# Optimization experiments

Measured on AMD Instinct MI355X. Metric: run time of the kernel, lower is better.

## Reference

```python
import jax, jax.numpy as jnp
import numpy as np

B, D = 256, 1024
MARGIN = 0.2  # contrastive margin


def setup_inputs() -> dict:
    key = jax.random.key(0)
    k_im, k_s = jax.random.split(key)
    im = jax.random.normal(k_im, (B, D), dtype=jnp.float32)
    # s viewed by the torch module as [1, B, B, D]; we pass it as [B, B, D]
    s = jax.random.normal(k_s, (B, B, D), dtype=jnp.float32)
    return {"im": im, "s": s}


def reference(im, s):
    # Torch code broadcasts to an O(B^3*D) intermediate then keeps only
    # M[i, j] = scores[j, i, j] = dot(im[j], s[i, j]).
    # We compute exactly those B^2 dot products directly.
    scores = jnp.einsum('jd,ijd->ij', im, s)  # [B, B]
    diag = jnp.diagonal(scores)               # [B]
    not_eye = ~jnp.eye(scores.shape[0], dtype=bool)
    # cost_s[i,j] = relu(margin + M[i,j] - M[i,i]); cost_im uses column diag
    cost_s = jnp.where(not_eye, jnp.maximum(MARGIN + scores - diag[:, None], 0.0), 0.0)
    cost_im = jnp.where(not_eye, jnp.maximum(MARGIN + scores - diag[None, :], 0.0), 0.0)
    # max_violation=True: hardest negative per row / per column
    cost_s = cost_s.max(axis=1)
    cost_im = cost_im.max(axis=0)
    return cost_s.sum() + cost_im.sum()
```

## Files before the change

### kernel.cpp

```cpp
#include <hip/hip_runtime.h>

#define BSZ 256
#define DDIM 1024
#define MARGIN 0.2f
#define WPB 4
#define PPW 8

__global__ __launch_bounds__(256) void scores_kernel(const float* __restrict__ im,
                                                     const float* __restrict__ s,
                                                     float* __restrict__ scores) {
    const int wave = threadIdx.x >> 6;
    const int lane = threadIdx.x & 63;
    const int w = blockIdx.x * WPB + wave;
    const int j = w & (BSZ - 1);
    const int iBase = (w >> 8) * PPW;

    const float4* ip = reinterpret_cast<const float4*>(im + (size_t)j * DDIM);
    float4 b0 = ip[0 * 64 + lane];
    float4 b1 = ip[1 * 64 + lane];
    float4 b2 = ip[2 * 64 + lane];
    float4 b3 = ip[3 * 64 + lane];

#pragma unroll
    for (int it = 0; it < PPW; ++it) {
        const int p = (iBase + it) * BSZ + j;
        const float4* sp = reinterpret_cast<const float4*>(s + (size_t)p * DDIM);
        float4 a0 = sp[0 * 64 + lane];
        float4 a1 = sp[1 * 64 + lane];
        float4 a2 = sp[2 * 64 + lane];
        float4 a3 = sp[3 * 64 + lane];
        float acc = a0.x * b0.x + a0.y * b0.y + a0.z * b0.z + a0.w * b0.w;
        acc += a1.x * b1.x + a1.y * b1.y + a1.z * b1.z + a1.w * b1.w;
        acc += a2.x * b2.x + a2.y * b2.y + a2.z * b2.z + a2.w * b2.w;
        acc += a3.x * b3.x + a3.y * b3.y + a3.z * b3.z + a3.w * b3.w;
#pragma unroll
        for (int off = 32; off > 0; off >>= 1) acc += __shfl_down(acc, off);
        if (lane == 0) scores[p] = acc;
    }
}

__global__ __launch_bounds__(256) void rowcol_kernel(const float* __restrict__ scores,
                                                     float* __restrict__ partial) {
    const int t = blockIdx.x;
    const int j = threadIdx.x;
    __shared__ float wr[4], wc[4];

    const float dg = scores[t * BSZ + t];
    float rowv = 0.0f, colv = 0.0f;
    if (j != t) {
        rowv = fmaxf(MARGIN + scores[t * BSZ + j] - dg, 0.0f);
        colv = fmaxf(MARGIN + scores[j * BSZ + t] - dg, 0.0f);
    }
#pragma unroll
    for (int off = 32; off > 0; off >>= 1) {
        rowv = fmaxf(rowv, __shfl_down(rowv, off));
        colv = fmaxf(colv, __shfl_down(colv, off));
    }
    const int wave = j >> 6;
    const int lane = j & 63;
    if (lane == 0) { wr[wave] = rowv; wc[wave] = colv; }
    __syncthreads();
    if (j == 0) {
        float rm = fmaxf(fmaxf(wr[0], wr[1]), fmaxf(wr[2], wr[3]));
        float cm = fmaxf(fmaxf(wc[0], wc[1]), fmaxf(wc[2], wc[3]));
        partial[t] = rm + cm;
    }
}

__global__ __launch_bounds__(256) void sum_kernel(const float* __restrict__ partial,
                                                  float* __restrict__ out) {
    const int t = threadIdx.x;
    __shared__ float wsum[4];
    float v = partial[t];
#pragma unroll
    for (int off = 32; off > 0; off >>= 1) v += __shfl_down(v, off);
    if ((t & 63) == 0) wsum[t >> 6] = v;
    __syncthreads();
    if (t == 0) out[0] = wsum[0] + wsum[1] + wsum[2] + wsum[3];
}

extern "C" void kernel_launch(void* const* d_in, const int* in_sizes, int n_in,
                              void* d_out, int out_size, void* d_ws, size_t ws_size,
                              hipStream_t stream) {
    const float* im = (const float*)d_in[0];
    const float* s  = (const float*)d_in[1];
    float* out = (float*)d_out;
    float* scores  = (float*)d_ws;
    float* partial = scores + BSZ * BSZ;

    const int nWaves = (BSZ * BSZ) / PPW;
    scores_kernel<<<nWaves / WPB, 256, 0, stream>>>(im, s, scores);
    rowcol_kernel<<<BSZ, 256, 0, stream>>>(scores, partial);
    sum_kernel<<<1, 256, 0, stream>>>(partial, out);
}
```

Before: 46.94 us.

## Fuse row/col and sum kernels via last-block atomic; use nontemporal loads

Merges the final sum kernel into the row/column epilogue using an atomic counter, so the last finishing block performs the global reduction. It also switches the streaming loads of s to nontemporal loads so they avoid polluting the cache. This removes one kernel launch but adds a memset on the stream and an atomic plus fences per block.

```diff
diff --git a/kernel.cpp b/kernel.cpp
--- a/kernel.cpp
+++ b/kernel.cpp
@@ -5,6 +5,8 @@
 #define MARGIN 0.2f
 #define WPB 4
 #define PPW 8
+
+typedef float f32x4 __attribute__((ext_vector_type(4)));
 
 __global__ __launch_bounds__(256) void scores_kernel(const float* __restrict__ im,
                                                      const float* __restrict__ s,
@@ -15,20 +17,20 @@
     const int j = w & (BSZ - 1);
     const int iBase = (w >> 8) * PPW;
 
-    const float4* ip = reinterpret_cast<const float4*>(im + (size_t)j * DDIM);
-    float4 b0 = ip[0 * 64 + lane];
-    float4 b1 = ip[1 * 64 + lane];
-    float4 b2 = ip[2 * 64 + lane];
-    float4 b3 = ip[3 * 64 + lane];
+    const f32x4* ip = reinterpret_cast<const f32x4*>(im + (size_t)j * DDIM);
+    f32x4 b0 = ip[0 * 64 + lane];
+    f32x4 b1 = ip[1 * 64 + lane];
+    f32x4 b2 = ip[2 * 64 + lane];
+    f32x4 b3 = ip[3 * 64 + lane];
 
 #pragma unroll
     for (int it = 0; it < PPW; ++it) {
         const int p = (iBase + it) * BSZ + j;
-        const float4* sp = reinterpret_cast<const float4*>(s + (size_t)p * DDIM);
-        float4 a0 = sp[0 * 64 + lane];
-        float4 a1 = sp[1 * 64 + lane];
-        float4 a2 = sp[2 * 64 + lane];
-        float4 a3 = sp[3 * 64 + lane];
+        const f32x4* sp = reinterpret_cast<const f32x4*>(s + (size_t)p * DDIM);
+        f32x4 a0 = __builtin_nontemporal_load(&sp[0 * 64 + lane]);
+        f32x4 a1 = __builtin_nontemporal_load(&sp[1 * 64 + lane]);
+        f32x4 a2 = __builtin_nontemporal_load(&sp[2 * 64 + lane]);
+        f32x4 a3 = __builtin_nontemporal_load(&sp[3 * 64 + lane]);
         float acc = a0.x * b0.x + a0.y * b0.y + a0.z * b0.z + a0.w * b0.w;
         acc += a1.x * b1.x + a1.y * b1.y + a1.z * b1.z + a1.w * b1.w;
         acc += a2.x * b2.x + a2.y * b2.y + a2.z * b2.z + a2.w * b2.w;
@@ -39,11 +41,16 @@
     }
 }
 
-__global__ __launch_bounds__(256) void rowcol_kernel(const float* __restrict__ scores,
-                                                     float* __restrict__ partial) {
+__global__ __launch_bounds__(256) void epilogue_kernel(const float* __restrict__ scores,
+                                                       float* __restrict__ partial,
+                                                       unsigned* __restrict__ counter,
+                                                       float* __restrict__ out) {
     const int t = blockIdx.x;
     const int j = threadIdx.x;
+    const int wave = j >> 6;
+    const int lane = j & 63;
     __shared__ float wr[4], wc[4];
+    __shared__ bool isLast;
 
     const float dg = scores[t * BSZ + t];
     float rowv = 0.0f, colv = 0.0f;
@@ -56,27 +63,28 @@
         rowv = fmaxf(rowv, __shfl_down(rowv, off));
         colv = fmaxf(colv, __shfl_down(colv, off));
     }
-    const int wave = j >> 6;
-    const int lane = j & 63;
     if (lane == 0) { wr[wave] = rowv; wc[wave] = colv; }
     __syncthreads();
     if (j == 0) {
         float rm = fmaxf(fmaxf(wr[0], wr[1]), fmaxf(wr[2], wr[3]));
         float cm = fmaxf(fmaxf(wc[0], wc[1]), fmaxf(wc[2], wc[3]));
         partial[t] = rm + cm;
+        __threadfence();
+        unsigned c = atomicAdd(counter, 1u);
+        isLast = (c == (unsigned)(gridDim.x - 1));
     }
-}
+    __syncthreads();
 
-__global__ __launch_bounds__(256) void sum_kernel(const float* __restrict__ partial,
-                                                  float* __restrict__ out) {
-    const int t = threadIdx.x;
-    __shared__ float wsum[4];
-    float v = partial[t];
+    if (isLast) {
+        __threadfence();
+        __shared__ float wsum[4];
+        float v = partial[j];
 #pragma unroll
-    for (int off = 32; off > 0; off >>= 1) v += __shfl_down(v, off);
-    if ((t & 63) == 0) wsum[t >> 6] = v;
-    __syncthreads();
-    if (t == 0) out[0] = wsum[0] + wsum[1] + wsum[2] + wsum[3];
+        for (int off = 32; off > 0; off >>= 1) v += __shfl_down(v, off);
+        if (lane == 0) wsum[wave] = v;
+        __syncthreads();
+        if (j == 0) out[0] = wsum[0] + wsum[1] + wsum[2] + wsum[3];
+    }
 }
 
 extern "C" void kernel_launch(void* const* d_in, const int* in_sizes, int n_in,
@@ -87,9 +95,11 @@
     float* out = (float*)d_out;
     float* scores  = (float*)d_ws;
     float* partial = scores + BSZ * BSZ;
+    unsigned* counter = (unsigned*)(partial + BSZ);
+
+    (void)hipMemsetAsync(counter, 0, sizeof(unsigned), stream);
 
     const int nWaves = (BSZ * BSZ) / PPW;
     scores_kernel<<<nWaves / WPB, 256, 0, stream>>>(im, s, scores);
-    rowcol_kernel<<<BSZ, 256, 0, stream>>>(scores, partial);
-    sum_kernel<<<1, 256, 0, stream>>>(partial, out);
+    epilogue_kernel<<<BSZ, 256, 0, stream>>>(scores, partial, counter, out);
 }
```

After: 57.05 us. 21.5% more time.
